# Kernel tuning notes

Measured on AMD Instinct MI355X. Metric: run time of the kernel, lower is better.

Reference implementation:

```python
import jax, jax.numpy as jnp
import numpy as np

B, S, D, H = 2, 1024, 1024, 16
DH = D // H            # dim per head = 64
MAX_REL = 32           # max relative positions
ROPE_BASE = 10000.0


def entmax15(X, axis=-1):
    """1.5-entmax with full sort (k=None path of the torch code)."""
    X = (X - jnp.max(X, axis=axis, keepdims=True)) / 2.0
    Xsrt = -jnp.sort(-X, axis=axis)                       # descending sort
    d = X.shape[axis]
    rho = jnp.arange(1, d + 1, dtype=X.dtype)             # broadcasts on last axis
    mean = jnp.cumsum(Xsrt, axis=axis) / rho
    mean_sq = jnp.cumsum(Xsrt * Xsrt, axis=axis) / rho
    ss = rho * (mean_sq - mean * mean)
    delta = (1.0 - ss) / rho
    tau = mean - jnp.sqrt(jnp.clip(delta, 0.0))
    support = jnp.sum(tau <= Xsrt, axis=axis, keepdims=True)
    tau_star = jnp.take_along_axis(tau, support - 1, axis=axis)
    Y = jnp.clip(X - tau_star, 0.0)
    return Y * Y


def _rope(x, cos, sin):
    # x: [B,S,H,DH]; cos/sin: [S, DH//2]; complex mult on (even,odd) pairs
    xe, xo = x[..., 0::2], x[..., 1::2]
    c = cos[None, :, None, :]
    s = sin[None, :, None, :]
    re = xe * c - xo * s
    im = xe * s + xo * c
    return jnp.stack([re, im], axis=-1).reshape(x.shape)


def setup_inputs() -> dict:
    key = jax.random.key(0)
    ks = jax.random.split(key, 10)
    sc = 0.02
    x = jax.random.normal(ks[0], (B, S, D), dtype=jnp.float32)
    w_q = jax.random.normal(ks[1], (D, D), dtype=jnp.float32) * sc
    w_k = jax.random.normal(ks[2], (D, D), dtype=jnp.float32) * sc
    w_v = jax.random.normal(ks[3], (D, D), dtype=jnp.float32) * sc
    w_o = jax.random.normal(ks[4], (D, D), dtype=jnp.float32) * sc
    b_q = jnp.zeros((D,), jnp.float32)
    b_k = jnp.zeros((D,), jnp.float32)
    b_v = jnp.zeros((D,), jnp.float32)
    b_o = jnp.zeros((D,), jnp.float32)
    rel_emb = jax.random.normal(ks[5], (2 * MAX_REL + 1, DH), dtype=jnp.float32) * sc
    inv_freq = 1.0 / (ROPE_BASE ** (np.arange(0, DH, 2, dtype=np.float32) / DH))
    ang = np.arange(S, dtype=np.float32)[:, None] * inv_freq[None, :]
    rope_cos = jnp.asarray(np.cos(ang), jnp.float32)
    rope_sin = jnp.asarray(np.sin(ang), jnp.float32)
    return {"x": x, "w_q": w_q, "b_q": b_q, "w_k": w_k, "b_k": b_k,
            "w_v": w_v, "b_v": b_v, "w_o": w_o, "b_o": b_o,
            "rel_emb": rel_emb, "rope_cos": rope_cos, "rope_sin": rope_sin}


def reference(x, w_q, b_q, w_k, b_k, w_v, b_v, w_o, b_o, rel_emb, rope_cos, rope_sin):
    # QKV projections -> [B,S,H,DH]
    q = (x @ w_q + b_q).reshape(B, S, H, DH)
    k = (x @ w_k + b_k).reshape(B, S, H, DH)
    v = (x @ w_v + b_v).reshape(B, S, H, DH).transpose(0, 2, 1, 3)  # [B,H,S,DH]
    # RoPE on q, k (applied in [B,S,H,DH] layout like the torch code)
    q = _rope(q, rope_cos, rope_sin).transpose(0, 2, 1, 3)  # [B,H,S,DH]
    k = _rope(k, rope_cos, rope_sin).transpose(0, 2, 1, 3)
    q = q / jnp.sqrt(jnp.asarray(DH, q.dtype))
    # content scores
    scores = jnp.einsum('bhqd,bhkd->bhqk', q, k)
    # relative position bias (Shaw et al.), shared embedding for keys & values
    r = jnp.arange(S)
    dist = jnp.clip(r[None, :] - r[:, None], -MAX_REL, MAX_REL) + MAX_REL  # [S,S]
    rel = rel_emb[dist]                                                   # [S,S,DH]
    scores = scores + jnp.einsum('bhqd,qkd->bhqk', q, rel)
    # sparse normalization
    attn = entmax15(scores, axis=-1)
    # context + relative-position values
    ctx = jnp.einsum('bhqk,bhkd->bhqd', attn, v) + jnp.einsum('bhqk,qkd->bhqd', attn, rel)
    out = ctx.transpose(0, 2, 1, 3).reshape(B, S, D) @ w_o + b_o
    return out
```

## Files before the change

kernel.cpp:

```cpp
#include <hip/hip_runtime.h>

typedef __attribute__((ext_vector_type(8))) short s8v;
typedef __attribute__((ext_vector_type(4))) short s4v;
typedef __attribute__((ext_vector_type(4))) float f4v;

__device__ __forceinline__ short f2bf(float f){
  union { float f; unsigned u; } v; v.f = f;
  unsigned r = v.u + 0x7fffu + ((v.u >> 16) & 1u);
  return (short)(r >> 16);
}
__device__ __forceinline__ float bf2f(short s){
  union { unsigned u; float f; } v; v.u = ((unsigned)(unsigned short)s) << 16; return v.f;
}
__device__ __forceinline__ void gload16(const void* g, void* l){
  __builtin_amdgcn_global_load_lds((const __attribute__((address_space(1))) unsigned int*)g,
                                   (__attribute__((address_space(3))) unsigned int*)l, 16, 0, 0);
}

__global__ __launch_bounds__(256) void prep_k(const float* __restrict__ w_q, const float* __restrict__ w_k,
                                              const float* __restrict__ w_v, const float* __restrict__ w_o,
                                              const float* __restrict__ x, const float* __restrict__ rel,
                                              short* __restrict__ wqkvT, short* __restrict__ woT,
                                              short* __restrict__ xb, short* __restrict__ relb,
                                              short* __restrict__ relT){
  int z = blockIdx.z;
  if (z < 4){
    __shared__ float t[64][65];
    const float* in = (z==0) ? w_q : (z==1) ? w_k : (z==2) ? w_v : w_o;
    short* out = (z==3) ? woT : (wqkvT + ((size_t)z<<20));
    int c0 = blockIdx.x*64, r0 = blockIdx.y*64;
    int tx = threadIdx.x & 63, ty = threadIdx.x >> 6;
    #pragma unroll
    for (int i=0;i<16;i++){ int r = ty + i*4; t[r][tx] = in[(size_t)(r0+r)*1024 + c0+tx]; }
    __syncthreads();
    #pragma unroll
    for (int i=0;i<16;i++){ int cc = ty + i*4; out[(size_t)(c0+cc)*1024 + r0+tx] = f2bf(t[tx][cc]); }
    if (z==3 && blockIdx.x==0 && blockIdx.y==0){
      for (int e = threadIdx.x; e < 65*64; e += 256){
        int j = e >> 6, d = e & 63;
        short bv = f2bf(rel[e]);
        relb[e] = bv;
        relT[d*72 + j] = bv;
      }
    }
  } else {
    int bid = (z-4)*256 + blockIdx.y*16 + blockIdx.x;
    int i = bid*256 + threadIdx.x;
    #pragma unroll
    for (int p=0;p<4;p++){
      int idx = p*131072 + i;
      f4v v = ((const f4v*)x)[idx];
      s4v o; o[0]=f2bf(v[0]); o[1]=f2bf(v[1]); o[2]=f2bf(v[2]); o[3]=f2bf(v[3]);
      ((s4v*)xb)[idx] = o;
    }
  }
}

__device__ __forceinline__ void gemm128_core(const short* __restrict__ A, const short* __restrict__ Bt,
                                             int m0, int n0, short* As, short* Bs, f4v acc[4][4]){
  int tid = threadIdx.x;
  int lane = tid & 63, wave = tid >> 6;
  int wr = wave >> 1, wc = wave & 1, g = lane >> 4, c = lane & 15;
  int lrow = lane >> 3, lcol = (lane & 7)*8;
  for (int k0 = 0; k0 < 1024; k0 += 64){
    #pragma unroll
    for (int p=0;p<4;p++){
      int r0 = wave*32 + p*8;
      int row = r0 + lrow;
      gload16(A  + (size_t)(m0+row)*1024 + k0 + lcol, &As[r0*64]);
      gload16(Bt + (size_t)(n0+row)*1024 + k0 + lcol, &Bs[r0*64]);
    }
    __syncthreads();
    #pragma unroll
    for (int ks=0;ks<2;ks++){
      s8v a[4], b[4];
      int pu = ks*32 + g*8;
      #pragma unroll
      for (int mi=0;mi<4;mi++) a[mi] = *(const s8v*)(&As[(wr*64 + mi*16 + c)*64 + pu]);
      #pragma unroll
      for (int ni=0;ni<4;ni++) b[ni] = *(const s8v*)(&Bs[(wc*64 + ni*16 + c)*64 + pu]);
      #pragma unroll
      for (int mi=0;mi<4;mi++)
        #pragma unroll
        for (int ni=0;ni<4;ni++)
          acc[mi][ni] = __builtin_amdgcn_mfma_f32_16x16x32_bf16(a[mi], b[ni], acc[mi][ni], 0,0,0);
    }
    __syncthreads();
  }
}

__global__ __launch_bounds__(256) void gemm_qkv_k(const short* __restrict__ A, const short* __restrict__ Bt,
                                                  const float* __restrict__ b_q, const float* __restrict__ b_k,
                                                  const float* __restrict__ b_v,
                                                  const float* __restrict__ cs, const float* __restrict__ sn,
                                                  short* __restrict__ Qb, short* __restrict__ Kb,
                                                  short* __restrict__ Vt){
  __shared__ __align__(16) char lbuf[33792];
  short* As = (short*)lbuf;
  short* Bs = (short*)(lbuf + 16384);
  short* st = (short*)lbuf;
  int flat = blockIdx.x;
  int swz = (flat & 7)*48 + (flat >> 3);
  int m0 = (swz / 24) * 128, n0 = (swz % 24) * 128;
  int lane = threadIdx.x & 63, wave = threadIdx.x >> 6;
  int wr = wave >> 1, wc = wave & 1, g = lane >> 4, c = lane & 15;
  f4v acc[4][4] = {};
  gemm128_core(A, Bt, m0, n0, As, Bs, acc);

  int sec = n0 >> 10;
  const float* bias = (sec==0) ? b_q : (sec==1) ? b_k : b_v;
  int b = m0 >> 10, s0 = m0 & 1023, hbase = (n0 & 1023) >> 6;
  #pragma unroll
  for (int mi=0;mi<4;mi++)
    #pragma unroll
    for (int ni=0;ni<4;ni++){
      int cl = wc*64 + ni*16 + c;
      int hcol = (n0 & 1023) + cl;
      float bi = bias[hcol];
      int d = hcol & 63, ifr = d >> 1;
      #pragma unroll
      for (int i=0;i<4;i++){
        int rl = wr*64 + mi*16 + g*4 + i;
        float v = acc[mi][ni][i] + bi;
        if (sec < 2){
          int s = s0 + rl;
          float co = cs[s*32 + ifr], si = sn[s*32 + ifr];
          float p = __shfl_xor(v, 1, 64);
          float o = (cl & 1) ? fmaf(p, si, v*co) : fmaf(v, co, -(p*si));
          if (sec == 0) o *= 0.125f;
          v = o;
        }
        st[rl*132 + cl] = f2bf(v);
      }
    }
  __syncthreads();
  if (sec < 2){
    short* dst = (sec==0) ? Qb : Kb;
    for (int e = threadIdx.x; e < 128*32; e += 256){
      int row = e >> 5, cl4 = (e & 31)*4;
      int h = hbase + (cl4 >> 6), d = cl4 & 63;
      s4v o = *(const s4v*)(&st[row*132 + cl4]);
      *(s4v*)(&dst[((size_t)(b*16+h)*1024 + s0 + row)*64 + d]) = o;
    }
  } else {
    for (int e = threadIdx.x; e < 128*32; e += 256){
      int cl = e >> 5, s4 = (e & 31)*4;
      int h = hbase + (cl >> 6), dl = cl & 63;
      s4v o;
      o[0] = st[(s4+0)*132 + cl]; o[1] = st[(s4+1)*132 + cl];
      o[2] = st[(s4+2)*132 + cl]; o[3] = st[(s4+3)*132 + cl];
      *(s4v*)(&Vt[(size_t)(b*16+h)*65536 + (size_t)dl*1024 + s0 + s4]) = o;
    }
  }
}

__global__ __launch_bounds__(256) void gemm_out_k(const short* __restrict__ A, const short* __restrict__ Bt,
                                                  const float* __restrict__ bias, float* __restrict__ C){
  __shared__ __align__(16) short As[128*64];
  __shared__ __align__(16) short Bs[128*64];
  int flat = blockIdx.x;
  int swz = (flat & 7)*16 + (flat >> 3);
  int n0 = (swz & 7)*128, m0 = (swz >> 3)*128;
  int lane = threadIdx.x & 63, wave = threadIdx.x >> 6;
  int wr = wave >> 1, wc = wave & 1, g = lane >> 4, c = lane & 15;
  f4v acc[4][4] = {};
  gemm128_core(A, Bt, m0, n0, As, Bs, acc);
  #pragma unroll
  for (int mi=0;mi<4;mi++)
    #pragma unroll
    for (int ni=0;ni<4;ni++){
      int col = n0 + wc*64 + ni*16 + c;
      float bi = bias[col];
      #pragma unroll
      for (int i=0;i<4;i++){
        int row = m0 + wr*64 + mi*16 + g*4 + i;
        C[(size_t)row*1024 + col] = acc[mi][ni][i] + bi;
      }
    }
}

#define ATPAD 1028
__global__ __launch_bounds__(256,4) void attn_fused_k(const short* __restrict__ Qb, const short* __restrict__ Kb,
                                                      const short* __restrict__ relb, const short* __restrict__ relT,
                                                      const short* __restrict__ Vt, short* __restrict__ ctxb){
  __shared__ __align__(16) short pb_b[16][66];
  __shared__ __align__(16) float wrow[16][68];
  __shared__ __align__(16) short attn_l[16][ATPAD];
  float2* red = (float2*)&pb_b[0][0];

  int lane = threadIdx.x & 63, wave = threadIdx.x >> 6;
  int g = lane >> 4, c = lane & 15;
  int flat = blockIdx.x;
  int swz = (flat & 7)*256 + (flat >> 3);
  int bh = swz >> 6, q0 = (swz & 63)*16;
  const short* Qh = Qb + (size_t)bh*65536;
  const short* Kh = Kb + (size_t)bh*65536;
  const short* Vh = Vt + (size_t)bh*65536;

  for (int e = threadIdx.x; e < 16*68; e += 256) ((float*)wrow)[e] = 0.f;

  s8v qa0 = *(const s8v*)(Qh + (q0+c)*64 + g*8);
  s8v qa1 = *(const s8v*)(Qh + (q0+c)*64 + 32 + g*8);

  {
    int ntile = (wave==3) ? 2 : 1;
    for (int t=0; t<ntile; t++){
      int jt = (t==0) ? wave : 4;
      int j = jt*16 + c;
      s8v rb0 = {}, rb1 = {};
      if (j < 65){
        rb0 = *(const s8v*)(relb + j*64 + g*8);
        rb1 = *(const s8v*)(relb + j*64 + 32 + g*8);
      }
      f4v pa = {};
      pa = __builtin_amdgcn_mfma_f32_16x16x32_bf16(qa0, rb0, pa, 0,0,0);
      pa = __builtin_amdgcn_mfma_f32_16x16x32_bf16(qa1, rb1, pa, 0,0,0);
      if (j < 65){
        #pragma unroll
        for (int i=0;i<4;i++) pb_b[g*4+i][j] = f2bf(pa[i]);
      }
    }
  }
  __syncthreads();

  int q = q0 + c;
  int kc0 = wave*256;
  int Lb = q0 - 32 - kc0;
  int Ub = q0 + 47 - kc0;
  float pb0  = bf2f(pb_b[c][0]);
  float pb64 = bf2f(pb_b[c][64]);
  f4v x[16];
  #pragma unroll
  for (int t=0;t<16;t++){
    f4v ini;
    if (t*16+15 <= Lb){ ini[0]=pb0; ini[1]=pb0; ini[2]=pb0; ini[3]=pb0; }
    else if (t*16 >= Ub){ ini[0]=pb64; ini[1]=pb64; ini[2]=pb64; ini[3]=pb64; }
    else {
      #pragma unroll
      for (int i=0;i<4;i++){
        int k = kc0 + t*16 + g*4 + i;
        int jj = min(max(k - q, -32), 32) + 32;
        ini[i] = bf2f(pb_b[c][jj]);
      }
    }
    const short* kp = Kh + (kc0 + t*16 + c)*64 + g*8;
    s8v ka0 = *(const s8v*)(kp);
    s8v ka1 = *(const s8v*)(kp + 32);
    ini = __builtin_amdgcn_mfma_f32_16x16x32_bf16(ka0, qa0, ini, 0,0,0);
    x[t] = __builtin_amdgcn_mfma_f32_16x16x32_bf16(ka1, qa1, ini, 0,0,0);
  }
  __syncthreads();

  f4v m4 = x[0];
  #pragma unroll
  for (int t=1;t<16;t++){
    m4[0]=fmaxf(m4[0],x[t][0]); m4[1]=fmaxf(m4[1],x[t][1]);
    m4[2]=fmaxf(m4[2],x[t][2]); m4[3]=fmaxf(m4[3],x[t][3]);
  }
  float mx = fmaxf(fmaxf(m4[0],m4[1]), fmaxf(m4[2],m4[3]));
  mx = fmaxf(mx, __shfl_xor(mx, 16, 64));
  mx = fmaxf(mx, __shfl_xor(mx, 32, 64));
  if (g == 0) red[wave*16 + c] = make_float2(mx, 0.f);
  __syncthreads();
  {
    float2 r0 = red[c], r1 = red[16+c], r2 = red[32+c], r3 = red[48+c];
    mx = fmaxf(fmaxf(r0.x, r1.x), fmaxf(r2.x, r3.x));
  }

  float theta = mx - 2.0f;
  for (int it=0; it<7; it++){
    f4v th4 = {theta, theta, theta, theta};
    f4v s1v = {0.f,0.f,0.f,0.f}, s2v = {0.f,0.f,0.f,0.f};
    #pragma unroll
    for (int t=0;t<16;t++){
      f4v d = x[t] - th4;
      f4v tt;
      tt[0]=fmaxf(d[0],0.f); tt[1]=fmaxf(d[1],0.f); tt[2]=fmaxf(d[2],0.f); tt[3]=fmaxf(d[3],0.f);
      s1v += tt;
      s2v += tt*tt;
    }
    float S1 = (s1v[0]+s1v[1])+(s1v[2]+s1v[3]);
    float S2 = (s2v[0]+s2v[1])+(s2v[2]+s2v[3]);
    S1 += __shfl_xor(S1, 16, 64); S2 += __shfl_xor(S2, 16, 64);
    S1 += __shfl_xor(S1, 32, 64); S2 += __shfl_xor(S2, 32, 64);
    int pp = (it+1)&1;
    if (g == 0) red[(pp*4 + wave)*16 + c] = make_float2(S1, S2);
    __syncthreads();
    float2 r0 = red[pp*64 + c], r1 = red[pp*64 + 16+c], r2 = red[pp*64 + 32+c], r3 = red[pp*64 + 48+c];
    S1 = (r0.x+r1.x)+(r2.x+r3.x);
    S2 = (r0.y+r1.y)+(r2.y+r3.y);
    theta += (S2 - 4.0f)/(2.0f*S1);
  }

  float w0p = 0.f, w64p = 0.f;
  {
    f4v th4 = {theta, theta, theta, theta};
    short* arow = &attn_l[c][kc0 + g*4];
    #pragma unroll
    for (int t=0;t<16;t++){
      f4v d = x[t] - th4;
      f4v tt;
      tt[0]=fmaxf(d[0],0.f); tt[1]=fmaxf(d[1],0.f); tt[2]=fmaxf(d[2],0.f); tt[3]=fmaxf(d[3],0.f);
      tt = tt*0.5f;
      f4v a = tt*tt;
      unsigned d0, d1;
      asm("v_cvt_pk_bf16_f32 %0, %1, %2" : "=v"(d0) : "v"(a[0]), "v"(a[1]));
      asm("v_cvt_pk_bf16_f32 %0, %1, %2" : "=v"(d1) : "v"(a[2]), "v"(a[3]));
      *(uint2*)(arow + t*16) = make_uint2(d0, d1);
      if (t*16+15 <= Lb)      w0p  += (a[0]+a[1])+(a[2]+a[3]);
      else if (t*16 >= Ub)    w64p += (a[0]+a[1])+(a[2]+a[3]);
      else {
        #pragma unroll
        for (int i=0;i<4;i++){
          int raw = kc0 + t*16 + g*4 + i - q;
          if (raw <= -32) w0p += a[i];
          else if (raw >= 32) w64p += a[i];
          else wrow[c][raw+32] = a[i];
        }
      }
    }
  }
  w0p += __shfl_xor(w0p, 16, 64); w64p += __shfl_xor(w64p, 16, 64);
  w0p += __shfl_xor(w0p, 32, 64); w64p += __shfl_xor(w64p, 32, 64);
  if (g == 0) red[wave*16 + c] = make_float2(w0p, w64p);
  __syncthreads();
  if (wave == 0 && g == 0){
    float2 r0 = red[c], r1 = red[16+c], r2 = red[32+c], r3 = red[48+c];
    wrow[c][0]  = (r0.x+r1.x)+(r2.x+r3.x);
    wrow[c][64] = (r0.y+r1.y)+(r2.y+r3.y);
  }
  __syncthreads();

  f4v acc = {};
  __builtin_amdgcn_s_setprio(1);
  #pragma unroll 8
  for (int kk=0; kk<32; kk++){
    s8v af = *(const s8v*)(&attn_l[c][kk*32 + g*8]);
    s8v bf = *(const s8v*)(Vh + (size_t)(wave*16+c)*1024 + kk*32 + g*8);
    acc = __builtin_amdgcn_mfma_f32_16x16x32_bf16(af, bf, acc, 0,0,0);
  }
  {
    const float* wp = &wrow[c][0];
    f4v A0 = *(const f4v*)(wp + g*8);
    f4v A1 = *(const f4v*)(wp + g*8 + 4);
    f4v A2 = *(const f4v*)(wp + 32 + g*8);
    f4v A3 = *(const f4v*)(wp + 32 + g*8 + 4);
    union { unsigned u[4]; s8v v; } W0, W1;
    asm("v_cvt_pk_bf16_f32 %0, %1, %2" : "=v"(W0.u[0]) : "v"(A0[0]), "v"(A0[1]));
    asm("v_cvt_pk_bf16_f32 %0, %1, %2" : "=v"(W0.u[1]) : "v"(A0[2]), "v"(A0[3]));
    asm("v_cvt_pk_bf16_f32 %0, %1, %2" : "=v"(W0.u[2]) : "v"(A1[0]), "v"(A1[1]));
    asm("v_cvt_pk_bf16_f32 %0, %1, %2" : "=v"(W0.u[3]) : "v"(A1[2]), "v"(A1[3]));
    asm("v_cvt_pk_bf16_f32 %0, %1, %2" : "=v"(W1.u[0]) : "v"(A2[0]), "v"(A2[1]));
    asm("v_cvt_pk_bf16_f32 %0, %1, %2" : "=v"(W1.u[1]) : "v"(A2[2]), "v"(A2[3]));
    asm("v_cvt_pk_bf16_f32 %0, %1, %2" : "=v"(W1.u[2]) : "v"(A3[0]), "v"(A3[1]));
    asm("v_cvt_pk_bf16_f32 %0, %1, %2" : "=v"(W1.u[3]) : "v"(A3[2]), "v"(A3[3]));
    s8v rb0 = *(const s8v*)(relT + (wave*16+c)*72 + g*8);
    s8v rb1 = *(const s8v*)(relT + (wave*16+c)*72 + 32 + g*8);
    acc = __builtin_amdgcn_mfma_f32_16x16x32_bf16(W0.v, rb0, acc, 0,0,0);
    acc = __builtin_amdgcn_mfma_f32_16x16x32_bf16(W1.v, rb1, acc, 0,0,0);
  }
  __builtin_amdgcn_s_setprio(0);
  int b = bh >> 4, h = bh & 15, d = wave*16 + c;
  float rl64 = bf2f(relT[d*72 + 64]);
  #pragma unroll
  for (int i=0;i<4;i++){
    int r = g*4+i;
    float s = acc[i] + wrow[r][64]*rl64;
    ctxb[((size_t)(b*1024 + q0 + r))*1024 + h*64 + d] = f2bf(s);
  }
}

extern "C" void kernel_launch(void* const* d_in, const int* in_sizes, int n_in,
                              void* d_out, int out_size, void* d_ws, size_t ws_size,
                              hipStream_t stream) {
  (void)in_sizes; (void)n_in; (void)out_size; (void)ws_size;
  const float* x    = (const float*)d_in[0];
  const float* w_q  = (const float*)d_in[1];
  const float* b_q  = (const float*)d_in[2];
  const float* w_k  = (const float*)d_in[3];
  const float* b_k  = (const float*)d_in[4];
  const float* w_v  = (const float*)d_in[5];
  const float* b_v  = (const float*)d_in[6];
  const float* w_o  = (const float*)d_in[7];
  const float* b_o  = (const float*)d_in[8];
  const float* rel  = (const float*)d_in[9];
  const float* rcos = (const float*)d_in[10];
  const float* rsin = (const float*)d_in[11];
  float* out = (float*)d_out;

  char* w = (char*)d_ws;
  short* xb    = (short*)(w);
  short* wqkvT = (short*)(w + ((size_t)4<<20));
  short* woT   = (short*)(w + ((size_t)10<<20));
  short* Qb    = (short*)(w + ((size_t)12<<20));
  short* Kb    = (short*)(w + ((size_t)16<<20));
  short* Vt    = (short*)(w + ((size_t)20<<20));
  short* ctxb  = (short*)(w + ((size_t)24<<20));
  short* relb  = (short*)(w + ((size_t)28<<20));
  short* relT  = (short*)(w + ((size_t)28<<20) + 65536);

  prep_k<<<dim3(16,16,6), 256, 0, stream>>>(w_q, w_k, w_v, w_o, x, rel, wqkvT, woT, xb, relb, relT);
  gemm_qkv_k<<<384, 256, 0, stream>>>(xb, wqkvT, b_q, b_k, b_v, rcos, rsin, Qb, Kb, Vt);
  attn_fused_k<<<2048, 256, 0, stream>>>(Qb, Kb, relb, relT, Vt, ctxb);
  gemm_out_k<<<128, 256, 0, stream>>>(ctxb, woT, b_o, out);
}
```

Before: 143.6 us.

## Solve entmax threshold per row within wavefronts, swizzle GEMM LDS, split PV accumulators

The entmax Newton iterations used to need a block-wide barrier every iteration. Each row is now staged as bf16 in LDS, so a 16-lane group owns one row and runs seven iterations using only shuffles. One full-precision Newton correction follows, and the LDS buffer is reused for the attention probabilities. Separately, the GEMM core XOR-swizzles its LDS columns to avoid bank conflicts, and the PV loop uses two accumulators to break the MFMA dependency chain. In exchange, register pressure rises (occupancy hint lowered from 4 to 3) and the bf16-staged iterations lose some precision before the final refinement.

```diff
diff --git a/kernel.cpp b/kernel.cpp
--- a/kernel.cpp
+++ b/kernel.cpp
@@ -12,6 +12,8 @@
 __device__ __forceinline__ float bf2f(short s){
   union { unsigned u; float f; } v; v.u = ((unsigned)(unsigned short)s) << 16; return v.f;
 }
+__device__ __forceinline__ float bflo(unsigned v){ union{unsigned u;float f;}w; w.u = v<<16; return w.f; }
+__device__ __forceinline__ float bfhi(unsigned v){ union{unsigned u;float f;}w; w.u = v & 0xffff0000u; return w.f; }
 __device__ __forceinline__ void gload16(const void* g, void* l){
   __builtin_amdgcn_global_load_lds((const __attribute__((address_space(1))) unsigned int*)g,
                                    (__attribute__((address_space(3))) unsigned int*)l, 16, 0, 0);
@@ -61,20 +63,20 @@
   int tid = threadIdx.x;
   int lane = tid & 63, wave = tid >> 6;
   int wr = wave >> 1, wc = wave & 1, g = lane >> 4, c = lane & 15;
-  int lrow = lane >> 3, lcol = (lane & 7)*8;
+  int lrow = lane >> 3;
+  int scol = ((lane & 7) ^ lrow) * 8;
   for (int k0 = 0; k0 < 1024; k0 += 64){
     #pragma unroll
     for (int p=0;p<4;p++){
       int r0 = wave*32 + p*8;
-      int row = r0 + lrow;
-      gload16(A  + (size_t)(m0+row)*1024 + k0 + lcol, &As[r0*64]);
-      gload16(Bt + (size_t)(n0+row)*1024 + k0 + lcol, &Bs[r0*64]);
+      gload16(A  + (size_t)(m0 + r0 + lrow)*1024 + k0 + scol, &As[r0*64]);
+      gload16(Bt + (size_t)(n0 + r0 + lrow)*1024 + k0 + scol, &Bs[r0*64]);
     }
     __syncthreads();
     #pragma unroll
     for (int ks=0;ks<2;ks++){
       s8v a[4], b[4];
-      int pu = ks*32 + g*8;
+      int pu = ((ks*4 + g) ^ (c & 7))*8;
       #pragma unroll
       for (int mi=0;mi<4;mi++) a[mi] = *(const s8v*)(&As[(wr*64 + mi*16 + c)*64 + pu]);
       #pragma unroll
@@ -179,14 +181,16 @@
     }
 }
 
+#define XSTR 1032
 #define ATPAD 1028
-__global__ __launch_bounds__(256,4) void attn_fused_k(const short* __restrict__ Qb, const short* __restrict__ Kb,
+__global__ __launch_bounds__(256,3) void attn_fused_k(const short* __restrict__ Qb, const short* __restrict__ Kb,
                                                       const short* __restrict__ relb, const short* __restrict__ relT,
                                                       const short* __restrict__ Vt, short* __restrict__ ctxb){
+  __shared__ __align__(16) short xbuf[16*XSTR];
+  __shared__ __align__(16) float wrow[16][68];
   __shared__ __align__(16) short pb_b[16][66];
-  __shared__ __align__(16) float wrow[16][68];
-  __shared__ __align__(16) short attn_l[16][ATPAD];
   float2* red = (float2*)&pb_b[0][0];
+  float* thb  = ((float*)&pb_b[0][0]) + 256;
 
   int lane = threadIdx.x & 63, wave = threadIdx.x >> 6;
   int g = lane >> 4, c = lane & 15;
@@ -267,9 +271,58 @@
     mx = fmaxf(fmaxf(r0.x, r1.x), fmaxf(r2.x, r3.x));
   }
 
-  float theta = mx - 2.0f;
+  {
+    f4v mx4 = {mx,mx,mx,mx};
+    #pragma unroll
+    for (int t=0;t<16;t++){
+      f4v u4 = x[t] - mx4;
+      unsigned d0,d1;
+      asm("v_cvt_pk_bf16_f32 %0, %1, %2" : "=v"(d0) : "v"(u4[0]), "v"(u4[1]));
+      asm("v_cvt_pk_bf16_f32 %0, %1, %2" : "=v"(d1) : "v"(u4[2]), "v"(u4[3]));
+      *(uint2*)(xbuf + c*XSTR + kc0 + t*16 + g*4) = make_uint2(d0,d1);
+    }
+  }
+  __syncthreads();
+
+  int rl = lane >> 4, rr = wave*4 + rl, cc = lane & 15;
+  f4v u[16];
+  #pragma unroll
+  for (int seg=0; seg<8; seg++){
+    uint4 pk = *(const uint4*)(xbuf + rr*XSTR + cc*8 + seg*128);
+    f4v a, b;
+    a[0]=bflo(pk.x); a[1]=bfhi(pk.x); a[2]=bflo(pk.y); a[3]=bfhi(pk.y);
+    b[0]=bflo(pk.z); b[1]=bfhi(pk.z); b[2]=bflo(pk.w); b[3]=bfhi(pk.w);
+    u[2*seg] = a; u[2*seg+1] = b;
+  }
+
+  float th = -2.0f;
+  #pragma unroll
   for (int it=0; it<7; it++){
-    f4v th4 = {theta, theta, theta, theta};
+    f4v th4 = {th,th,th,th};
+    f4v s1v = {0.f,0.f,0.f,0.f}, s2v = {0.f,0.f,0.f,0.f};
+    #pragma unroll
+    for (int t=0;t<16;t++){
+      f4v d = u[t] - th4;
+      f4v tt;
+      tt[0]=fmaxf(d[0],0.f); tt[1]=fmaxf(d[1],0.f); tt[2]=fmaxf(d[2],0.f); tt[3]=fmaxf(d[3],0.f);
+      s1v += tt;
+      s2v += tt*tt;
+    }
+    float S1 = (s1v[0]+s1v[1])+(s1v[2]+s1v[3]);
+    float S2 = (s2v[0]+s2v[1])+(s2v[2]+s2v[3]);
+    S1 += __shfl_xor(S1, 1, 64); S2 += __shfl_xor(S2, 1, 64);
+    S1 += __shfl_xor(S1, 2, 64); S2 += __shfl_xor(S2, 2, 64);
+    S1 += __shfl_xor(S1, 4, 64); S2 += __shfl_xor(S2, 4, 64);
+    S1 += __shfl_xor(S1, 8, 64); S2 += __shfl_xor(S2, 8, 64);
+    th += (S2 - 4.0f)/(2.0f*S1);
+  }
+  if ((lane & 15) == 0) thb[rr] = th;
+  __syncthreads();
+
+  float theta;
+  {
+    float thx = mx + thb[c];
+    f4v th4 = {thx,thx,thx,thx};
     f4v s1v = {0.f,0.f,0.f,0.f}, s2v = {0.f,0.f,0.f,0.f};
     #pragma unroll
     for (int t=0;t<16;t++){
@@ -283,19 +336,18 @@
     float S2 = (s2v[0]+s2v[1])+(s2v[2]+s2v[3]);
     S1 += __shfl_xor(S1, 16, 64); S2 += __shfl_xor(S2, 16, 64);
     S1 += __shfl_xor(S1, 32, 64); S2 += __shfl_xor(S2, 32, 64);
-    int pp = (it+1)&1;
-    if (g == 0) red[(pp*4 + wave)*16 + c] = make_float2(S1, S2);
+    if (g == 0) red[64 + wave*16 + c] = make_float2(S1, S2);
     __syncthreads();
-    float2 r0 = red[pp*64 + c], r1 = red[pp*64 + 16+c], r2 = red[pp*64 + 32+c], r3 = red[pp*64 + 48+c];
+    float2 r0 = red[64+c], r1 = red[64+16+c], r2 = red[64+32+c], r3 = red[64+48+c];
     S1 = (r0.x+r1.x)+(r2.x+r3.x);
     S2 = (r0.y+r1.y)+(r2.y+r3.y);
-    theta += (S2 - 4.0f)/(2.0f*S1);
+    theta = thx + (S2 - 4.0f)/(2.0f*S1);
   }
 
   float w0p = 0.f, w64p = 0.f;
   {
     f4v th4 = {theta, theta, theta, theta};
-    short* arow = &attn_l[c][kc0 + g*4];
+    short* arow = xbuf + c*ATPAD + kc0 + g*4;
     #pragma unroll
     for (int t=0;t<16;t++){
       f4v d = x[t] - th4;
@@ -331,14 +383,18 @@
   }
   __syncthreads();
 
-  f4v acc = {};
+  f4v acc0 = {}, acc1 = {};
   __builtin_amdgcn_s_setprio(1);
-  #pragma unroll 8
-  for (int kk=0; kk<32; kk++){
-    s8v af = *(const s8v*)(&attn_l[c][kk*32 + g*8]);
-    s8v bf = *(const s8v*)(Vh + (size_t)(wave*16+c)*1024 + kk*32 + g*8);
-    acc = __builtin_amdgcn_mfma_f32_16x16x32_bf16(af, bf, acc, 0,0,0);
-  }
+  #pragma unroll
+  for (int kk=0; kk<32; kk+=2){
+    s8v af0 = *(const s8v*)(&xbuf[c*ATPAD + kk*32 + g*8]);
+    s8v bf0 = *(const s8v*)(Vh + (size_t)(wave*16+c)*1024 + kk*32 + g*8);
+    acc0 = __builtin_amdgcn_mfma_f32_16x16x32_bf16(af0, bf0, acc0, 0,0,0);
+    s8v af1 = *(const s8v*)(&xbuf[c*ATPAD + (kk+1)*32 + g*8]);
+    s8v bf1 = *(const s8v*)(Vh + (size_t)(wave*16+c)*1024 + (kk+1)*32 + g*8);
+    acc1 = __builtin_amdgcn_mfma_f32_16x16x32_bf16(af1, bf1, acc1, 0,0,0);
+  }
+  f4v acc = acc0 + acc1;
   {
     const float* wp = &wrow[c][0];
     f4v A0 = *(const f4v*)(wp + g*8);
```

Measured after the change: 158.9 us. 10.7% more time.

## Keep attention probs in registers, split PV over key chunks, swizzle GEMM LDS

Applied to the files above, without the earlier changes.

The attention kernel no longer writes the full 16x1024 bf16 probability row block to LDS. Each wave keeps its own key-chunk probabilities in registers, rebuilds MFMA A-fragments with lane shuffles, and computes partial contexts for all 64 head dims. Partials are reduced across waves through a small shared buffer. Dropping the large LDS array allows a higher occupancy bound (6 blocks per CU instead of 4), at the cost of more registers, extra shuffles, a cross-wave reduction, and rel-bias MFMAs done only by wave 0. Separately, the GEMM LDS tile uses an XOR swizzle on 16-byte columns to reduce bank conflicts.

```diff
diff --git a/kernel.cpp b/kernel.cpp
--- a/kernel.cpp
+++ b/kernel.cpp
@@ -61,20 +61,20 @@
   int tid = threadIdx.x;
   int lane = tid & 63, wave = tid >> 6;
   int wr = wave >> 1, wc = wave & 1, g = lane >> 4, c = lane & 15;
-  int lrow = lane >> 3, lcol = (lane & 7)*8;
+  int lrow = lane >> 3;
+  int scol = ((lane & 7) ^ lrow) * 8;
   for (int k0 = 0; k0 < 1024; k0 += 64){
     #pragma unroll
     for (int p=0;p<4;p++){
       int r0 = wave*32 + p*8;
-      int row = r0 + lrow;
-      gload16(A  + (size_t)(m0+row)*1024 + k0 + lcol, &As[r0*64]);
-      gload16(Bt + (size_t)(n0+row)*1024 + k0 + lcol, &Bs[r0*64]);
+      gload16(A  + (size_t)(m0 + r0 + lrow)*1024 + k0 + scol, &As[r0*64]);
+      gload16(Bt + (size_t)(n0 + r0 + lrow)*1024 + k0 + scol, &Bs[r0*64]);
     }
     __syncthreads();
     #pragma unroll
     for (int ks=0;ks<2;ks++){
       s8v a[4], b[4];
-      int pu = ks*32 + g*8;
+      int pu = ((ks*4 + g) ^ (c & 7))*8;
       #pragma unroll
       for (int mi=0;mi<4;mi++) a[mi] = *(const s8v*)(&As[(wr*64 + mi*16 + c)*64 + pu]);
       #pragma unroll
@@ -179,14 +179,15 @@
     }
 }
 
-#define ATPAD 1028
-__global__ __launch_bounds__(256,4) void attn_fused_k(const short* __restrict__ Qb, const short* __restrict__ Kb,
+#define PSTR 68
+__global__ __launch_bounds__(256,6) void attn_fused_k(const short* __restrict__ Qb, const short* __restrict__ Kb,
                                                       const short* __restrict__ relb, const short* __restrict__ relT,
                                                       const short* __restrict__ Vt, short* __restrict__ ctxb){
-  __shared__ __align__(16) short pb_b[16][66];
   __shared__ __align__(16) float wrow[16][68];
-  __shared__ __align__(16) short attn_l[16][ATPAD];
-  float2* red = (float2*)&pb_b[0][0];
+  __shared__ __align__(16) char  ureg[4*16*PSTR*4];
+  short (*pb_b)[66] = (short(*)[66])ureg;
+  float2* red  = (float2*)ureg;
+  float*  part = (float*)ureg;
 
   int lane = threadIdx.x & 63, wave = threadIdx.x >> 6;
   int g = lane >> 4, c = lane & 15;
@@ -292,10 +293,10 @@
     theta += (S2 - 4.0f)/(2.0f*S1);
   }
 
+  uint2 pk[16];
   float w0p = 0.f, w64p = 0.f;
   {
     f4v th4 = {theta, theta, theta, theta};
-    short* arow = &attn_l[c][kc0 + g*4];
     #pragma unroll
     for (int t=0;t<16;t++){
       f4v d = x[t] - th4;
@@ -306,7 +307,7 @@
       unsigned d0, d1;
       asm("v_cvt_pk_bf16_f32 %0, %1, %2" : "=v"(d0) : "v"(a[0]), "v"(a[1]));
       asm("v_cvt_pk_bf16_f32 %0, %1, %2" : "=v"(d1) : "v"(a[2]), "v"(a[3]));
-      *(uint2*)(arow + t*16) = make_uint2(d0, d1);
+      pk[t] = make_uint2(d0, d1);
       if (t*16+15 <= Lb)      w0p  += (a[0]+a[1])+(a[2]+a[3]);
       else if (t*16 >= Ub)    w64p += (a[0]+a[1])+(a[2]+a[3]);
       else {
@@ -331,15 +332,8 @@
   }
   __syncthreads();
 
-  f4v acc = {};
-  __builtin_amdgcn_s_setprio(1);
-  #pragma unroll 8
-  for (int kk=0; kk<32; kk++){
-    s8v af = *(const s8v*)(&attn_l[c][kk*32 + g*8]);
-    s8v bf = *(const s8v*)(Vh + (size_t)(wave*16+c)*1024 + kk*32 + g*8);
-    acc = __builtin_amdgcn_mfma_f32_16x16x32_bf16(af, bf, acc, 0,0,0);
-  }
-  {
+  f4v acc[4] = {};
+  if (wave == 0){
     const float* wp = &wrow[c][0];
     f4v A0 = *(const f4v*)(wp + g*8);
     f4v A1 = *(const f4v*)(wp + g*8 + 4);
@@ -354,19 +348,66 @@
     asm("v_cvt_pk_bf16_f32 %0, %1, %2" : "=v"(W1.u[1]) : "v"(A2[2]), "v"(A2[3]));
     asm("v_cvt_pk_bf16_f32 %0, %1, %2" : "=v"(W1.u[2]) : "v"(A3[0]), "v"(A3[1]));
     asm("v_cvt_pk_bf16_f32 %0, %1, %2" : "=v"(W1.u[3]) : "v"(A3[2]), "v"(A3[3]));
-    s8v rb0 = *(const s8v*)(relT + (wave*16+c)*72 + g*8);
-    s8v rb1 = *(const s8v*)(relT + (wave*16+c)*72 + 32 + g*8);
-    acc = __builtin_amdgcn_mfma_f32_16x16x32_bf16(W0.v, rb0, acc, 0,0,0);
-    acc = __builtin_amdgcn_mfma_f32_16x16x32_bf16(W1.v, rb1, acc, 0,0,0);
+    #pragma unroll
+    for (int dt=0; dt<4; dt++){
+      s8v rb0 = *(const s8v*)(relT + (dt*16+c)*72 + g*8);
+      s8v rb1 = *(const s8v*)(relT + (dt*16+c)*72 + 32 + g*8);
+      acc[dt] = __builtin_amdgcn_mfma_f32_16x16x32_bf16(W0.v, rb0, acc[dt], 0,0,0);
+      acc[dt] = __builtin_amdgcn_mfma_f32_16x16x32_bf16(W1.v, rb1, acc[dt], 0,0,0);
+    }
+  }
+  __builtin_amdgcn_s_setprio(1);
+  {
+    int srcA = ((g & 1) << 5) + c;
+    bool hiT = (g >> 1);
+    #pragma unroll
+    for (int kk=0; kk<8; kk++){
+      uint2 pkA = pk[2*kk], pkB = pk[2*kk+1];
+      unsigned va0 = __shfl((int)pkA.x, srcA, 64);
+      unsigned va1 = __shfl((int)pkA.y, srcA, 64);
+      unsigned va2 = __shfl((int)pkA.x, srcA+16, 64);
+      unsigned va3 = __shfl((int)pkA.y, srcA+16, 64);
+      unsigned vb0 = __shfl((int)pkB.x, srcA, 64);
+      unsigned vb1 = __shfl((int)pkB.y, srcA, 64);
+      unsigned vb2 = __shfl((int)pkB.x, srcA+16, 64);
+      unsigned vb3 = __shfl((int)pkB.y, srcA+16, 64);
+      union { unsigned u[4]; s8v v; } Af;
+      Af.u[0] = hiT ? vb0 : va0;
+      Af.u[1] = hiT ? vb1 : va1;
+      Af.u[2] = hiT ? vb2 : va2;
+      Af.u[3] = hiT ? vb3 : va3;
+      #pragma unroll
+      for (int dt=0; dt<4; dt++){
+        s8v bf = *(const s8v*)(Vh + (size_t)(dt*16+c)*1024 + kc0 + kk*32 + g*8);
+        acc[dt] = __builtin_amdgcn_mfma_f32_16x16x32_bf16(Af.v, bf, acc[dt], 0,0,0);
+      }
+    }
   }
   __builtin_amdgcn_s_setprio(0);
-  int b = bh >> 4, h = bh & 15, d = wave*16 + c;
-  float rl64 = bf2f(relT[d*72 + 64]);
+
   #pragma unroll
-  for (int i=0;i<4;i++){
-    int r = g*4+i;
-    float s = acc[i] + wrow[r][64]*rl64;
-    ctxb[((size_t)(b*1024 + q0 + r))*1024 + h*64 + d] = f2bf(s);
+  for (int dt=0; dt<4; dt++)
+    #pragma unroll
+    for (int i=0;i<4;i++)
+      part[(wave*16 + g*4 + i)*PSTR + dt*16 + c] = acc[dt][i];
+  __syncthreads();
+
+  {
+    int r = threadIdx.x >> 4, dg = (threadIdx.x & 15)*4;
+    f4v s0 = *(const f4v*)&part[(0*16 + r)*PSTR + dg];
+    f4v s1 = *(const f4v*)&part[(1*16 + r)*PSTR + dg];
+    f4v s2 = *(const f4v*)&part[(2*16 + r)*PSTR + dg];
+    f4v s3 = *(const f4v*)&part[(3*16 + r)*PSTR + dg];
+    f4v sm = (s0 + s1) + (s2 + s3);
+    float wr64 = wrow[r][64];
+    int b = bh >> 4, h = bh & 15;
+    s4v o;
+    #pragma unroll
+    for (int j=0;j<4;j++){
+      float v = sm[j] + wr64 * bf2f(relT[(dg+j)*72 + 64]);
+      o[j] = f2bf(v);
+    }
+    *(s4v*)(&ctxb[((size_t)(b*1024 + q0 + r))*1024 + h*64 + dg]) = o;
   }
 }
 
```

After: 157.5 us. 9.7% more time.

## Shrink GEMM tiles to 128x64 and XOR-swizzle LDS layout

Applied to the files above, without the earlier changes.

Both projection GEMMs now use 128x64 output tiles instead of 128x128, doubling the grid (768 and 256 blocks) so the 256 compute units are better filled on these small GEMMs. The LDS tile layout gets an XOR swizzle on the 16-byte column chunks, applied at load and at read time, to cut bank conflicts on the MFMA operand reads. The QKV epilogue is simplified because each tile now covers exactly one head. Smaller tiles lower arithmetic intensity per block and increase redundant A-tile loads.

```diff
diff --git a/kernel.cpp b/kernel.cpp
--- a/kernel.cpp
+++ b/kernel.cpp
@@ -56,33 +56,37 @@
   }
 }
 
-__device__ __forceinline__ void gemm128_core(const short* __restrict__ A, const short* __restrict__ Bt,
-                                             int m0, int n0, short* As, short* Bs, f4v acc[4][4]){
+__device__ __forceinline__ void gemm12864_core(const short* __restrict__ A, const short* __restrict__ Bt,
+                                               int m0, int n0, short* As, short* Bs, f4v acc[4][2]){
   int tid = threadIdx.x;
   int lane = tid & 63, wave = tid >> 6;
   int wr = wave >> 1, wc = wave & 1, g = lane >> 4, c = lane & 15;
-  int lrow = lane >> 3, lcol = (lane & 7)*8;
+  int lrow = lane >> 3;
+  int scol = ((lane & 7) ^ lrow) * 8;
   for (int k0 = 0; k0 < 1024; k0 += 64){
     #pragma unroll
     for (int p=0;p<4;p++){
       int r0 = wave*32 + p*8;
-      int row = r0 + lrow;
-      gload16(A  + (size_t)(m0+row)*1024 + k0 + lcol, &As[r0*64]);
-      gload16(Bt + (size_t)(n0+row)*1024 + k0 + lcol, &Bs[r0*64]);
+      gload16(A + (size_t)(m0 + r0 + lrow)*1024 + k0 + scol, &As[r0*64]);
+    }
+    #pragma unroll
+    for (int p=0;p<2;p++){
+      int r0 = wave*16 + p*8;
+      gload16(Bt + (size_t)(n0 + r0 + lrow)*1024 + k0 + scol, &Bs[r0*64]);
     }
     __syncthreads();
     #pragma unroll
     for (int ks=0;ks<2;ks++){
-      s8v a[4], b[4];
-      int pu = ks*32 + g*8;
+      s8v a[4], b[2];
+      int pu = ((ks*4 + g) ^ (c & 7))*8;
       #pragma unroll
       for (int mi=0;mi<4;mi++) a[mi] = *(const s8v*)(&As[(wr*64 + mi*16 + c)*64 + pu]);
       #pragma unroll
-      for (int ni=0;ni<4;ni++) b[ni] = *(const s8v*)(&Bs[(wc*64 + ni*16 + c)*64 + pu]);
+      for (int ni=0;ni<2;ni++) b[ni] = *(const s8v*)(&Bs[(wc*32 + ni*16 + c)*64 + pu]);
       #pragma unroll
       for (int mi=0;mi<4;mi++)
         #pragma unroll
-        for (int ni=0;ni<4;ni++)
+        for (int ni=0;ni<2;ni++)
           acc[mi][ni] = __builtin_amdgcn_mfma_f32_16x16x32_bf16(a[mi], b[ni], acc[mi][ni], 0,0,0);
     }
     __syncthreads();
@@ -95,29 +99,28 @@
                                                   const float* __restrict__ cs, const float* __restrict__ sn,
                                                   short* __restrict__ Qb, short* __restrict__ Kb,
                                                   short* __restrict__ Vt){
-  __shared__ __align__(16) char lbuf[33792];
+  __shared__ __align__(16) char lbuf[24576];
   short* As = (short*)lbuf;
   short* Bs = (short*)(lbuf + 16384);
   short* st = (short*)lbuf;
   int flat = blockIdx.x;
-  int swz = (flat & 7)*48 + (flat >> 3);
-  int m0 = (swz / 24) * 128, n0 = (swz % 24) * 128;
+  int swz = (flat & 7)*96 + (flat >> 3);
+  int m0 = (swz / 48) * 128, n0 = (swz % 48) * 64;
   int lane = threadIdx.x & 63, wave = threadIdx.x >> 6;
   int wr = wave >> 1, wc = wave & 1, g = lane >> 4, c = lane & 15;
-  f4v acc[4][4] = {};
-  gemm128_core(A, Bt, m0, n0, As, Bs, acc);
+  f4v acc[4][2] = {};
+  gemm12864_core(A, Bt, m0, n0, As, Bs, acc);
 
   int sec = n0 >> 10;
   const float* bias = (sec==0) ? b_q : (sec==1) ? b_k : b_v;
-  int b = m0 >> 10, s0 = m0 & 1023, hbase = (n0 & 1023) >> 6;
+  int b = m0 >> 10, s0 = m0 & 1023, h0 = (n0 & 1023) >> 6;
   #pragma unroll
   for (int mi=0;mi<4;mi++)
     #pragma unroll
-    for (int ni=0;ni<4;ni++){
-      int cl = wc*64 + ni*16 + c;
-      int hcol = (n0 & 1023) + cl;
-      float bi = bias[hcol];
-      int d = hcol & 63, ifr = d >> 1;
+    for (int ni=0;ni<2;ni++){
+      int cl = wc*32 + ni*16 + c;
+      float bi = bias[(n0 & 1023) + cl];
+      int ifr = cl >> 1;
       #pragma unroll
       for (int i=0;i<4;i++){
         int rl = wr*64 + mi*16 + g*4 + i;
@@ -130,26 +133,26 @@
           if (sec == 0) o *= 0.125f;
           v = o;
         }
-        st[rl*132 + cl] = f2bf(v);
+        st[rl*66 + cl] = f2bf(v);
       }
     }
   __syncthreads();
   if (sec < 2){
     short* dst = (sec==0) ? Qb : Kb;
-    for (int e = threadIdx.x; e < 128*32; e += 256){
-      int row = e >> 5, cl4 = (e & 31)*4;
-      int h = hbase + (cl4 >> 6), d = cl4 & 63;
-      s4v o = *(const s4v*)(&st[row*132 + cl4]);
-      *(s4v*)(&dst[((size_t)(b*16+h)*1024 + s0 + row)*64 + d]) = o;
+    size_t base = ((size_t)(b*16+h0)*1024 + s0)*64;
+    for (int e = threadIdx.x; e < 128*16; e += 256){
+      int row = e >> 4, cl4 = (e & 15)*4;
+      s4v o = *(const s4v*)(&st[row*66 + cl4]);
+      *(s4v*)(&dst[base + (size_t)row*64 + cl4]) = o;
     }
   } else {
-    for (int e = threadIdx.x; e < 128*32; e += 256){
-      int cl = e >> 5, s4 = (e & 31)*4;
-      int h = hbase + (cl >> 6), dl = cl & 63;
+    size_t base = (size_t)(b*16+h0)*65536;
+    for (int e = threadIdx.x; e < 64*32; e += 256){
+      int d = e >> 5, s4 = (e & 31)*4;
       s4v o;
-      o[0] = st[(s4+0)*132 + cl]; o[1] = st[(s4+1)*132 + cl];
-      o[2] = st[(s4+2)*132 + cl]; o[3] = st[(s4+3)*132 + cl];
-      *(s4v*)(&Vt[(size_t)(b*16+h)*65536 + (size_t)dl*1024 + s0 + s4]) = o;
+      o[0] = st[(s4+0)*66 + d]; o[1] = st[(s4+1)*66 + d];
+      o[2] = st[(s4+2)*66 + d]; o[3] = st[(s4+3)*66 + d];
+      *(s4v*)(&Vt[base + (size_t)d*1024 + s0 + s4]) = o;
     }
   }
 }
@@ -157,19 +160,19 @@
 __global__ __launch_bounds__(256) void gemm_out_k(const short* __restrict__ A, const short* __restrict__ Bt,
                                                   const float* __restrict__ bias, float* __restrict__ C){
   __shared__ __align__(16) short As[128*64];
-  __shared__ __align__(16) short Bs[128*64];
+  __shared__ __align__(16) short Bs[64*64];
   int flat = blockIdx.x;
-  int swz = (flat & 7)*16 + (flat >> 3);
-  int n0 = (swz & 7)*128, m0 = (swz >> 3)*128;
+  int swz = (flat & 7)*32 + (flat >> 3);
+  int m0 = (swz >> 4)*128, n0 = (swz & 15)*64;
   int lane = threadIdx.x & 63, wave = threadIdx.x >> 6;
   int wr = wave >> 1, wc = wave & 1, g = lane >> 4, c = lane & 15;
-  f4v acc[4][4] = {};
-  gemm128_core(A, Bt, m0, n0, As, Bs, acc);
+  f4v acc[4][2] = {};
+  gemm12864_core(A, Bt, m0, n0, As, Bs, acc);
   #pragma unroll
   for (int mi=0;mi<4;mi++)
     #pragma unroll
-    for (int ni=0;ni<4;ni++){
-      int col = n0 + wc*64 + ni*16 + c;
+    for (int ni=0;ni<2;ni++){
+      int col = n0 + wc*32 + ni*16 + c;
       float bi = bias[col];
       #pragma unroll
       for (int i=0;i<4;i++){
@@ -400,7 +403,7 @@
   short* relT  = (short*)(w + ((size_t)28<<20) + 65536);
 
   prep_k<<<dim3(16,16,6), 256, 0, stream>>>(w_q, w_k, w_v, w_o, x, rel, wqkvT, woT, xb, relb, relT);
-  gemm_qkv_k<<<384, 256, 0, stream>>>(xb, wqkvT, b_q, b_k, b_v, rcos, rsin, Qb, Kb, Vt);
+  gemm_qkv_k<<<768, 256, 0, stream>>>(xb, wqkvT, b_q, b_k, b_v, rcos, rsin, Qb, Kb, Vt);
   attn_fused_k<<<2048, 256, 0, stream>>>(Qb, Kb, relb, relT, Vt, ctxb);
-  gemm_out_k<<<128, 256, 0, stream>>>(ctxb, woT, b_o, out);
-}
+  gemm_out_k<<<256, 256, 0, stream>>>(ctxb, woT, b_o, out);
+}
```

New measurement: 125.5 us. 12.6% less time.
